# Performance work log

Measured on AMD Instinct MI355X. Metric: run time of the kernel, lower is better.

Reference implementation:

```python
import jax, jax.numpy as jnp
import numpy as np

BANDWIDTH = 1.0


def setup_inputs() -> dict:
    key = jax.random.key(0)
    k1, k2 = jax.random.split(key)
    test_Xs = jax.random.normal(k1, (4096, 16), dtype=jnp.float32)
    train_Xs = jax.random.normal(k2, (8192, 16), dtype=jnp.float32)
    return {"test_Xs": test_Xs, "train_Xs": train_Xs}


def reference(test_Xs, train_Xs):
    n, d = train_Xs.shape
    h = jnp.float32(BANDWIDTH)
    # log normalization constant of n Gaussian kernels with bandwidth h in d dims
    Z = 0.5 * d * jnp.log(2 * jnp.float32(np.pi)) + d * jnp.log(h) + jnp.log(jnp.float32(n))
    # diffs: [n_test, n_train, d]
    diffs = (test_Xs[:, None, :] - train_Xs[None, :, :]) / h
    log_exp = -0.5 * jnp.sum(diffs * diffs, axis=-1)  # [n_test, n_train]
    return jax.scipy.special.logsumexp(log_exp - Z, axis=-1)  # [n_test]
```

## Files before the change

### kernel.cpp

```cpp
#include <hip/hip_runtime.h>
#include <math.h>

#define LOG2E 1.4426950408889634f
#define LN2   0.6931471805599453f
#define NW 16
#define CH 64

typedef short short8 __attribute__((ext_vector_type(8)));
typedef float f32x16 __attribute__((ext_vector_type(16)));

__device__ inline unsigned int cvtpk_bf16(float lo, float hi) {
    unsigned int r;
    asm("v_cvt_pk_bf16_f32 %0, %1, %2" : "=v"(r) : "v"(lo), "v"(hi));
    return r;
}

__global__ __launch_bounds__(1024, 4) void kde_fused(
    const float* __restrict__ testX, const float* __restrict__ trainX,
    float* __restrict__ out, int nTest, int nTrain, int nch, float Z)
{
    const int tid  = threadIdx.x;
    const int lane = tid & 63;
    const int w    = tid >> 6;
    const int c    = lane & 31;
    const int half = lane >> 5;
    const int rowBase = blockIdx.x * 16;

    __shared__ short8 stage[NW][2][2 * CH];
    __shared__ float  wbuf[NW][2][CH];
    __shared__ float  xnbuf[16];
    __shared__ __align__(16) float red2[NW][32][20];
    __shared__ __align__(16) float red3[16][68];

    const int mrow = min(rowBase + (c & 15), nTest - 1);
    const float4* xp = (const float4*)(testX + (size_t)mrow * 16) + half * 2;
    float4 xa = xp[0], xb = xp[1];
    float f0 = xa.x*LOG2E, f1 = xa.y*LOG2E, f2 = xa.z*LOG2E, f3 = xa.w*LOG2E;
    float f4 = xb.x*LOG2E, f5 = xb.y*LOG2E, f6 = xb.z*LOG2E, f7 = xb.w*LOG2E;
    float pn = ((f0*f0 + f1*f1) + (f2*f2 + f3*f3))
             + ((f4*f4 + f5*f5) + (f6*f6 + f7*f7));
    float xn2 = (pn + __shfl_xor(pn, 32)) * (0.5f / LOG2E);
    union { unsigned int u[4]; short8 s; } au;
    au.u[0] = cvtpk_bf16(f0, f1);
    au.u[1] = cvtpk_bf16(f2, f3);
    au.u[2] = cvtpk_bf16(f4, f5);
    au.u[3] = cvtpk_bf16(f6, f7);
    const short8 afrag = au.s;
    if (w == 0 && half == 0 && c < 16) xnbuf[c] = xn2;

    const int nMax = nTrain - 1;
    const int tb   = w * nch * CH;
    const int rdU  = (c * 2 + half) ^ ((c >> 2) & 7);
    const int pp   = lane & 31, ti64 = lane >> 5;
    const int u0s  = (pp * 2 + 0) ^ ((pp >> 2) & 7);
    const int u1s  = (pp * 2 + 1) ^ ((pp >> 2) & 7);

    float rs[8];
    #pragma unroll
    for (int i = 0; i < 8; ++i) rs[i] = 0.0f;
    const f32x16 zc = {0.f,0.f,0.f,0.f,0.f,0.f,0.f,0.f,
                       0.f,0.f,0.f,0.f,0.f,0.f,0.f,0.f};

    #define LOADPT(CHN, Q0,Q1,Q2,Q3,VLD) {                                    \
        int gi = tb + (CHN) * CH + lane;                                      \
        VLD = (gi <= nMax);                                                   \
        const float4* p = (const float4*)(trainX + (size_t)min(gi, nMax)*16); \
        Q0 = p[0]; Q1 = p[1]; Q2 = p[2]; Q3 = p[3]; }

    #define WRITEPT(Q0,Q1,Q2,Q3,VLD,B) {                                      \
        float nrm = ((Q0.x*Q0.x + Q0.y*Q0.y) + (Q0.z*Q0.z + Q0.w*Q0.w))       \
                  + ((Q1.x*Q1.x + Q1.y*Q1.y) + (Q1.z*Q1.z + Q1.w*Q1.w))       \
                  + ((Q2.x*Q2.x + Q2.y*Q2.y) + (Q2.z*Q2.z + Q2.w*Q2.w))       \
                  + ((Q3.x*Q3.x + Q3.y*Q3.y) + (Q3.z*Q3.z + Q3.w*Q3.w));      \
        float wvv = (VLD) ? __builtin_amdgcn_exp2f(-0.5f*LOG2E*nrm) : 0.0f;   \
        union { unsigned int u[4]; short8 s; } bu0, bu1;                      \
        bu0.u[0]=cvtpk_bf16(Q0.x,Q0.y); bu0.u[1]=cvtpk_bf16(Q0.z,Q0.w);       \
        bu0.u[2]=cvtpk_bf16(Q1.x,Q1.y); bu0.u[3]=cvtpk_bf16(Q1.z,Q1.w);       \
        bu1.u[0]=cvtpk_bf16(Q2.x,Q2.y); bu1.u[1]=cvtpk_bf16(Q2.z,Q2.w);       \
        bu1.u[2]=cvtpk_bf16(Q3.x,Q3.y); bu1.u[3]=cvtpk_bf16(Q3.z,Q3.w);       \
        stage[w][B][ti64 * 64 + u0s] = bu0.s;                                 \
        stage[w][B][ti64 * 64 + u1s] = bu1.s;                                 \
        wbuf[w][B][lane] = wvv; }

    #define INNER(B) {                                                        \
        short8 bf0 = stage[w][B][rdU];                                        \
        short8 bf1 = stage[w][B][64 + rdU];                                   \
        float  wt0 = wbuf[w][B][c];                                           \
        float  wt1 = wbuf[w][B][32 + c];                                      \
        f32x16 d0 = __builtin_amdgcn_mfma_f32_32x32x16_bf16(afrag,bf0,zc,0,0,0);\
        f32x16 d1 = __builtin_amdgcn_mfma_f32_32x32x16_bf16(afrag,bf1,zc,0,0,0);\
        _Pragma("unroll")                                                     \
        for (int r = 0; r < 8; ++r)                                           \
            rs[r] += __builtin_amdgcn_exp2f(d0[r]) * wt0;                     \
        _Pragma("unroll")                                                     \
        for (int r = 0; r < 8; ++r)                                           \
            rs[r] += __builtin_amdgcn_exp2f(d1[r]) * wt1; }

    float4 ra0,ra1,ra2,ra3, rb0,rb1,rb2,rb3;
    bool vA, vB;
    LOADPT(0, ra0,ra1,ra2,ra3, vA);
    LOADPT(1, rb0,rb1,rb2,rb3, vB);
    WRITEPT(ra0,ra1,ra2,ra3, vA, 0);
    int ch = 0;
    for (; ch + 2 < nch; ch += 2) {
        INNER(0);
        LOADPT(ch + 2, ra0,ra1,ra2,ra3, vA);
        WRITEPT(rb0,rb1,rb2,rb3, vB, 1);
        INNER(1);
        LOADPT(ch + 3, rb0,rb1,rb2,rb3, vB);
        WRITEPT(ra0,ra1,ra2,ra3, vA, 0);
    }
    INNER(0);
    WRITEPT(rb0,rb1,rb2,rb3, vB, 1);
    INNER(1);

    #undef LOADPT
    #undef WRITEPT
    #undef INNER

    {
        float4 v0 = make_float4(rs[0], rs[1], rs[2], rs[3]);
        float4 v1 = make_float4(rs[4], rs[5], rs[6], rs[7]);
        *(float4*)&red2[w][c][half * 4]     = v0;
        *(float4*)&red2[w][c][8 + half * 4] = v1;
    }
    __syncthreads();

    {
        int row = tid & 15, seg = tid >> 4;
        int wv2 = seg >> 2, cb = (seg & 3) * 8;
        float s = 0.0f;
        #pragma unroll
        for (int i = 0; i < 8; ++i) s += red2[wv2][cb + i][row];
        red3[row][seg] = s;
    }
    __syncthreads();

    if (tid < 16) {
        int row = rowBase + tid;
        if (row < nTest) {
            float s = 0.0f;
            #pragma unroll
            for (int k = 0; k < 16; ++k) {
                float4 v = *(const float4*)&red3[tid][k * 4];
                s += (v.x + v.y) + (v.z + v.w);
            }
            out[row] = __logf(s) - xnbuf[tid] * LN2 - Z;
        }
    }
}

extern "C" void kernel_launch(void* const* d_in, const int* in_sizes, int n_in,
                              void* d_out, int out_size, void* d_ws, size_t ws_size,
                              hipStream_t stream) {
    const float* testX  = (const float*)d_in[0];
    const float* trainX = (const float*)d_in[1];
    float* out = (float*)d_out;

    const int D = 16;
    const int nTest  = in_sizes[0] / D;
    const int nTrain = in_sizes[1] / D;

    const float Z = 0.5f * (float)D * logf(2.0f * (float)M_PI) + logf((float)nTrain);

    int nch = (nTrain + NW * CH - 1) / (NW * CH);
    nch = (nch + 1) & ~1;
    const int grid = (nTest + 15) / 16;

    kde_fused<<<grid, 1024, 0, stream>>>(testX, trainX, out, nTest, nTrain, nch, Z);
}
```

Measured before the change: 15.80 us.

## Load train fragments directly into MFMA registers, dropping LDS staging

Each lane now loads its own half of a training point straight from global memory in the layout the MFMA B operand expects, and builds the bf16 fragment in registers. This removes the per-wave LDS stage and weight buffers along with their swizzled writes and reads. Each tile now covers 32 training points, and the point norm is combined with a cross-half shuffle. In exchange there is redundant per-tile conversion and norm work, plus global loads that are less coalesced, 32 bytes per lane, with both lane halves reading the same points.

New measurement: 15.56 us. Within noise of the previous version (-1.5%).

```diff
diff --git a/kernel.cpp b/kernel.cpp
--- a/kernel.cpp
+++ b/kernel.cpp
@@ -4,7 +4,6 @@
 #define LOG2E 1.4426950408889634f
 #define LN2   0.6931471805599453f
 #define NW 16
-#define CH 64
 
 typedef short short8 __attribute__((ext_vector_type(8)));
 typedef float f32x16 __attribute__((ext_vector_type(16)));
@@ -17,7 +16,7 @@
 
 __global__ __launch_bounds__(1024, 4) void kde_fused(
     const float* __restrict__ testX, const float* __restrict__ trainX,
-    float* __restrict__ out, int nTest, int nTrain, int nch, float Z)
+    float* __restrict__ out, int nTest, int nTrain, int nt, float Z)
 {
     const int tid  = threadIdx.x;
     const int lane = tid & 63;
@@ -26,9 +25,7 @@
     const int half = lane >> 5;
     const int rowBase = blockIdx.x * 16;
 
-    __shared__ short8 stage[NW][2][2 * CH];
-    __shared__ float  wbuf[NW][2][CH];
-    __shared__ float  xnbuf[16];
+    __shared__ float xnbuf[16];
     __shared__ __align__(16) float red2[NW][32][20];
     __shared__ __align__(16) float red3[16][68];
 
@@ -37,9 +34,9 @@
     float4 xa = xp[0], xb = xp[1];
     float f0 = xa.x*LOG2E, f1 = xa.y*LOG2E, f2 = xa.z*LOG2E, f3 = xa.w*LOG2E;
     float f4 = xb.x*LOG2E, f5 = xb.y*LOG2E, f6 = xb.z*LOG2E, f7 = xb.w*LOG2E;
-    float pn = ((f0*f0 + f1*f1) + (f2*f2 + f3*f3))
-             + ((f4*f4 + f5*f5) + (f6*f6 + f7*f7));
-    float xn2 = (pn + __shfl_xor(pn, 32)) * (0.5f / LOG2E);
+    float pnx = ((f0*f0 + f1*f1) + (f2*f2 + f3*f3))
+              + ((f4*f4 + f5*f5) + (f6*f6 + f7*f7));
+    float xn2 = (pnx + __shfl_xor(pnx, 32)) * (0.5f / LOG2E);
     union { unsigned int u[4]; short8 s; } au;
     au.u[0] = cvtpk_bf16(f0, f1);
     au.u[1] = cvtpk_bf16(f2, f3);
@@ -49,11 +46,8 @@
     if (w == 0 && half == 0 && c < 16) xnbuf[c] = xn2;
 
     const int nMax = nTrain - 1;
-    const int tb   = w * nch * CH;
-    const int rdU  = (c * 2 + half) ^ ((c >> 2) & 7);
-    const int pp   = lane & 31, ti64 = lane >> 5;
-    const int u0s  = (pp * 2 + 0) ^ ((pp >> 2) & 7);
-    const int u1s  = (pp * 2 + 1) ^ ((pp >> 2) & 7);
+    const int tb   = w * nt * 32;
+    const float* tbase = trainX + (size_t)half * 8;
 
     float rs[8];
     #pragma unroll
@@ -61,62 +55,37 @@
     const f32x16 zc = {0.f,0.f,0.f,0.f,0.f,0.f,0.f,0.f,
                        0.f,0.f,0.f,0.f,0.f,0.f,0.f,0.f};
 
-    #define LOADPT(CHN, Q0,Q1,Q2,Q3,VLD) {                                    \
-        int gi = tb + (CHN) * CH + lane;                                      \
-        VLD = (gi <= nMax);                                                   \
-        const float4* p = (const float4*)(trainX + (size_t)min(gi, nMax)*16); \
-        Q0 = p[0]; Q1 = p[1]; Q2 = p[2]; Q3 = p[3]; }
+    #define LOADT(T, QA, QB) {                                                \
+        int gi = tb + (T) * 32 + c;                                           \
+        const float4* p = (const float4*)(tbase + (size_t)min(gi, nMax)*16);  \
+        QA = p[0]; QB = p[1]; }
 
-    #define WRITEPT(Q0,Q1,Q2,Q3,VLD,B) {                                      \
-        float nrm = ((Q0.x*Q0.x + Q0.y*Q0.y) + (Q0.z*Q0.z + Q0.w*Q0.w))       \
-                  + ((Q1.x*Q1.x + Q1.y*Q1.y) + (Q1.z*Q1.z + Q1.w*Q1.w))       \
-                  + ((Q2.x*Q2.x + Q2.y*Q2.y) + (Q2.z*Q2.z + Q2.w*Q2.w))       \
-                  + ((Q3.x*Q3.x + Q3.y*Q3.y) + (Q3.z*Q3.z + Q3.w*Q3.w));      \
-        float wvv = (VLD) ? __builtin_amdgcn_exp2f(-0.5f*LOG2E*nrm) : 0.0f;   \
-        union { unsigned int u[4]; short8 s; } bu0, bu1;                      \
-        bu0.u[0]=cvtpk_bf16(Q0.x,Q0.y); bu0.u[1]=cvtpk_bf16(Q0.z,Q0.w);       \
-        bu0.u[2]=cvtpk_bf16(Q1.x,Q1.y); bu0.u[3]=cvtpk_bf16(Q1.z,Q1.w);       \
-        bu1.u[0]=cvtpk_bf16(Q2.x,Q2.y); bu1.u[1]=cvtpk_bf16(Q2.z,Q2.w);       \
-        bu1.u[2]=cvtpk_bf16(Q3.x,Q3.y); bu1.u[3]=cvtpk_bf16(Q3.z,Q3.w);       \
-        stage[w][B][ti64 * 64 + u0s] = bu0.s;                                 \
-        stage[w][B][ti64 * 64 + u1s] = bu1.s;                                 \
-        wbuf[w][B][lane] = wvv; }
-
-    #define INNER(B) {                                                        \
-        short8 bf0 = stage[w][B][rdU];                                        \
-        short8 bf1 = stage[w][B][64 + rdU];                                   \
-        float  wt0 = wbuf[w][B][c];                                           \
-        float  wt1 = wbuf[w][B][32 + c];                                      \
-        f32x16 d0 = __builtin_amdgcn_mfma_f32_32x32x16_bf16(afrag,bf0,zc,0,0,0);\
-        f32x16 d1 = __builtin_amdgcn_mfma_f32_32x32x16_bf16(afrag,bf1,zc,0,0,0);\
+    #define PROC(T, QA, QB) {                                                 \
+        float pn = ((QA.x*QA.x + QA.y*QA.y) + (QA.z*QA.z + QA.w*QA.w))        \
+                 + ((QB.x*QB.x + QB.y*QB.y) + (QB.z*QB.z + QB.w*QB.w));       \
+        float fn = pn + __shfl_xor(pn, 32);                                   \
+        float wt = (tb + (T) * 32 + c <= nMax)                                \
+                 ? __builtin_amdgcn_exp2f(-0.5f * LOG2E * fn) : 0.0f;         \
+        union { unsigned int u[4]; short8 s; } bu;                            \
+        bu.u[0] = cvtpk_bf16(QA.x, QA.y);                                     \
+        bu.u[1] = cvtpk_bf16(QA.z, QA.w);                                     \
+        bu.u[2] = cvtpk_bf16(QB.x, QB.y);                                     \
+        bu.u[3] = cvtpk_bf16(QB.z, QB.w);                                     \
+        f32x16 d = __builtin_amdgcn_mfma_f32_32x32x16_bf16(afrag,bu.s,zc,0,0,0);\
         _Pragma("unroll")                                                     \
         for (int r = 0; r < 8; ++r)                                           \
-            rs[r] += __builtin_amdgcn_exp2f(d0[r]) * wt0;                     \
-        _Pragma("unroll")                                                     \
-        for (int r = 0; r < 8; ++r)                                           \
-            rs[r] += __builtin_amdgcn_exp2f(d1[r]) * wt1; }
+            rs[r] += __builtin_amdgcn_exp2f(d[r]) * wt; }
 
-    float4 ra0,ra1,ra2,ra3, rb0,rb1,rb2,rb3;
-    bool vA, vB;
-    LOADPT(0, ra0,ra1,ra2,ra3, vA);
-    LOADPT(1, rb0,rb1,rb2,rb3, vB);
-    WRITEPT(ra0,ra1,ra2,ra3, vA, 0);
-    int ch = 0;
-    for (; ch + 2 < nch; ch += 2) {
-        INNER(0);
-        LOADPT(ch + 2, ra0,ra1,ra2,ra3, vA);
-        WRITEPT(rb0,rb1,rb2,rb3, vB, 1);
-        INNER(1);
-        LOADPT(ch + 3, rb0,rb1,rb2,rb3, vB);
-        WRITEPT(ra0,ra1,ra2,ra3, vA, 0);
+    float4 a0,b0,a1,b1;
+    LOADT(0, a0, b0);
+    for (int t = 0; t < nt; t += 2) {
+        LOADT(t + 1, a1, b1);
+        PROC(t, a0, b0);
+        if (t + 2 < nt) LOADT(t + 2, a0, b0);
+        PROC(t + 1, a1, b1);
     }
-    INNER(0);
-    WRITEPT(rb0,rb1,rb2,rb3, vB, 1);
-    INNER(1);
-
-    #undef LOADPT
-    #undef WRITEPT
-    #undef INNER
+    #undef LOADT
+    #undef PROC
 
     {
         float4 v0 = make_float4(rs[0], rs[1], rs[2], rs[3]);
@@ -163,9 +132,9 @@
 
     const float Z = 0.5f * (float)D * logf(2.0f * (float)M_PI) + logf((float)nTrain);
 
-    int nch = (nTrain + NW * CH - 1) / (NW * CH);
-    nch = (nch + 1) & ~1;
+    int nt = (nTrain + NW * 32 - 1) / (NW * 32);
+    nt = (nt + 1) & ~1;
     const int grid = (nTest + 15) / 16;
 
-    kde_fused<<<grid, 1024, 0, stream>>>(testX, trainX, out, nTest, nTrain, nch, Z);
+    kde_fused<<<grid, 1024, 0, stream>>>(testX, trainX, out, nTest, nTrain, nt, Z);
 }
```
